# Optimization experiments

Measured on AMD Instinct MI355X. Metric: run time of the kernel, lower is better.

The kernel has to match this reference:

```python
import jax, jax.numpy as jnp
import numpy as np

B, P, K = 8, 2048, 20          # graphs, points per graph, fps samples per graph
N, M = B * P, B * K            # total points, total fps points
C_IN, C_OUT = 64, 128
EPS = 1e-5                     # BatchNorm eps (torch default)


def _linear(x, W, b):
    return x @ W.T + b


def _bn(x, g, b):
    # training-mode BatchNorm1d: batch stats over rows (biased variance)
    m = jnp.mean(x, axis=0)
    v = jnp.var(x, axis=0)
    return g * (x - m) * jax.lax.rsqrt(v + EPS) + b


def _mlp(x, W1, b1, g1, be1, W2, b2, g2, be2):
    h = jax.nn.relu(_bn(_linear(x, W1, b1), g1, be1))
    return jax.nn.relu(_bn(_linear(h, W2, b2), g2, be2))


def setup_inputs() -> dict:
    key = jax.random.key(0)
    ks = jax.random.split(key, 16)
    rng = np.random.default_rng(0)
    # sorted FPS indices: 20 distinct points per graph (matches indices.sort())
    fps = np.sort(rng.choice(P, size=(B, K), replace=False), axis=1)
    fps = fps + np.arange(B)[:, None] * P

    s = 0.05
    inp = {
        "x": jax.random.normal(ks[0], (N, C_IN), jnp.float32),
        "pos": jax.random.normal(ks[1], (N, 3), jnp.float32),
        # q/k/v projections
        "Wq": jax.random.normal(ks[2], (C_OUT, C_IN)) * s, "bq": jnp.zeros((C_OUT,)),
        "Wk": jax.random.normal(ks[3], (C_OUT, C_IN)) * s, "bk": jnp.zeros((C_OUT,)),
        "Wv": jax.random.normal(ks[4], (C_OUT, C_IN)) * s, "bv": jnp.zeros((C_OUT,)),
        # pos MLP: Linear(3,C) BN ReLU Linear(C,C) BN ReLU
        "pW1": jax.random.normal(ks[5], (C_OUT, 3)) * s, "pb1": jnp.zeros((C_OUT,)),
        "pg1": jnp.ones((C_OUT,)), "pbe1": jnp.zeros((C_OUT,)),
        "pW2": jax.random.normal(ks[6], (C_OUT, C_OUT)) * s, "pb2": jnp.zeros((C_OUT,)),
        "pg2": jnp.ones((C_OUT,)), "pbe2": jnp.zeros((C_OUT,)),
        # attn MLP: Linear(C,C) BN ReLU Linear(C,C) BN ReLU
        "aW1": jax.random.normal(ks[7], (C_OUT, C_OUT)) * s, "ab1": jnp.zeros((C_OUT,)),
        "ag1": jnp.ones((C_OUT,)), "abe1": jnp.zeros((C_OUT,)),
        "aW2": jax.random.normal(ks[8], (C_OUT, C_OUT)) * s, "ab2": jnp.zeros((C_OUT,)),
        "ag2": jnp.ones((C_OUT,)), "abe2": jnp.zeros((C_OUT,)),
        "fps_idx": jnp.asarray(fps.reshape(-1), jnp.int32),
        "batch": jnp.repeat(jnp.arange(B, dtype=jnp.int32), P),
    }
    return inp


def reference(x, pos, Wq, bq, Wk, bk, Wv, bv,
              pW1, pb1, pg1, pbe1, pW2, pb2, pg2, pbe2,
              aW1, ab1, ag1, abe1, aW2, ab2, ag2, abe2,
              fps_idx, batch):
    # --- FPS gather + knn(k=1, batched) ---
    fps_pos = pos[fps_idx]                          # [M,3]
    pos_b = pos.reshape(B, P, 3)
    fpos_b = fps_pos.reshape(B, K, 3)
    d2 = jnp.sum((pos_b[:, :, None, :] - fpos_b[:, None, :, :]) ** 2, -1)  # [B,P,K]
    nn_local = jnp.argmin(d2, axis=-1)              # [B,P] nearest fps per point
    e1 = (nn_local + jnp.arange(B)[:, None] * K).reshape(-1)  # [N] global fps idx
    ek1 = 1.0 / (1.0 + 5.0 * jnp.min(d2, axis=-1).reshape(-1))  # [N]

    # --- scatter-mean of kernel-weighted x/pos onto fps nodes ---
    seg = jax.ops.segment_sum
    cnt = jnp.maximum(seg(jnp.ones((N,), x.dtype), e1, num_segments=M), 1.0)[:, None]
    fps_x = seg(ek1[:, None] * x, e1, num_segments=M) / cnt       # [M,C_IN]
    fps_pos = seg(ek1[:, None] * pos, e1, num_segments=M) / cnt   # [M,3]

    # --- q/k/v projections ---
    x_q = _linear(x, Wq, bq)        # [N,C]
    x_k = _linear(fps_x, Wk, bk)    # [M,C]
    x_v = _linear(fps_x, Wv, bv)    # [M,C]

    # --- all-pairs (local point, global fps-in-same-graph) edges: E = N*K ---
    rel = (pos_b[:, :, None, :] - fps_pos.reshape(B, K, 3)[:, None, :, :])
    rel = rel.reshape(N * K, 3)                                   # [E,3]
    delta = _mlp(rel, pW1, pb1, pg1, pbe1, pW2, pb2, pg2, pbe2)   # [E,C]

    qmk = (x_q.reshape(B, P, 1, C_OUT) - x_k.reshape(B, 1, K, C_OUT))
    qmk = qmk.reshape(N * K, C_OUT)                               # [E,C]
    alpha = _mlp(qmk + delta, aW1, ab1, ag1, abe1, aW2, ab2, ag2, abe2)
    # segment softmax over each local point's K edges, per channel
    alpha = jax.nn.softmax(alpha.reshape(B, P, K, C_OUT), axis=2)

    vpd = x_v.reshape(B, 1, K, C_OUT) + delta.reshape(B, P, K, C_OUT)
    out = jnp.sum(vpd * alpha, axis=2).reshape(N, C_OUT)          # scatter-add
    return out
```

## Files before the change

### kernel.cpp

```cpp
#include <hip/hip_runtime.h>
#include <hip/hip_bf16.h>
#include <stdint.h>

#define B_ 8
#define P_ 2048
#define K_ 20
#define N_ (B_*P_)
#define M_ (B_*K_)
#define C 128
#define E_ (N_*K_)
#define EPS_ 1e-5f

typedef unsigned short u16;
typedef unsigned int u32;
typedef __attribute__((ext_vector_type(8))) short short8;
typedef __attribute__((ext_vector_type(4))) float floatx4;

__device__ __forceinline__ float bf2f(u16 u){
    union { u32 i; float f; } v; v.i = ((u32)u) << 16; return v.f;
}
__device__ __forceinline__ u16 f2bf(float f){
    union { float f; u32 i; } v; v.f = f;
    u32 r = ((v.i >> 16) & 1u) + 0x7fffu;
    return (u16)((v.i + r) >> 16);
}
__device__ __forceinline__ u32 pkbf(float a, float b){
    union { __hip_bfloat162 h; u32 u; } cv;
    cv.h = __float22bfloat162_rn(make_float2(a, b));
    return cv.u;
}

__global__ __launch_bounds__(256)
void prep_weights(const float* __restrict__ Wq, const float* __restrict__ bq,
                  const float* __restrict__ Wk, const float* __restrict__ bk,
                  const float* __restrict__ aW1, const float* __restrict__ ab1,
                  const float* __restrict__ pW2, const float* __restrict__ aW2,
                  float* __restrict__ Cq, float* __restrict__ Ck,
                  float* __restrict__ dq, float* __restrict__ dk,
                  u16* __restrict__ Wb0, u16* __restrict__ Wb1, u16* __restrict__ Wb2)
{
    int tid = threadIdx.x, blk = blockIdx.x;
    if (blk < 32) {
        int idx = blk*256 + tid; int o = idx >> 6, i = idx & 63;
        float s = 0.f;
        for (int cc = 0; cc < 128; ++cc) s = fmaf(aW1[o*128+cc], Wq[cc*64+i], s);
        Cq[idx] = s;
    } else if (blk < 64) {
        int idx = (blk-32)*256 + tid; int o = idx >> 6, i = idx & 63;
        float s = 0.f;
        for (int cc = 0; cc < 128; ++cc) s = fmaf(aW1[o*128+cc], Wk[cc*64+i], s);
        Ck[idx] = s;
    } else if (blk == 64) {
        if (tid < 128) {
            float s = ab1[tid];
            for (int cc = 0; cc < 128; ++cc) s = fmaf(aW1[tid*128+cc], bq[cc], s);
            dq[tid] = s;
        } else {
            int o = tid - 128;
            float s = 0.f;
            for (int cc = 0; cc < 128; ++cc) s = fmaf(aW1[o*128+cc], bk[cc], s);
            dk[o] = s;
        }
    } else {
        const float* src = (blk == 65) ? pW2 : (blk == 66) ? aW1 : aW2;
        u16* dst = (blk == 65) ? Wb0 : (blk == 66) ? Wb1 : Wb2;
        for (int s = tid; s < 2048; s += 256) {
            int ln = s & 63, ks = (s >> 6) & 3, ct = s >> 8;
            int Ls = ln & 15, qs = ln >> 4;
            const float* sp = src + (ct*16+Ls)*C + ks*32 + qs*8;
            #pragma unroll
            for (int j = 0; j < 8; ++j) dst[s*8+j] = f2bf(sp[j]);
        }
    }
}

__global__ __launch_bounds__(64)
void knn_scatter(const float* __restrict__ pos, const float* __restrict__ x,
                 const int* __restrict__ fps_idx, float* __restrict__ gacc,
                 float* __restrict__ posmom)
{
    __shared__ float fpos[K_][3];
    __shared__ float accL[K_*68];
    int lane = threadIdx.x;
    int b = blockIdx.x >> 5;
    if (lane < K_*3) {
        int k = lane / 3, d = lane - k*3;
        fpos[k][d] = pos[fps_idx[b*K_+k]*3 + d];
    }
    for (int i = lane; i < K_*68; i += 64) accL[i] = 0.f;
    __syncthreads();

    int wbase = blockIdx.x*64;
    int p = wbase + lane;
    float px = pos[p*3], py = pos[p*3+1], pz = pos[p*3+2];
    float best = 1e30f; int kb = 0;
    #pragma unroll
    for (int k = 0; k < K_; ++k) {
        float dx = px - fpos[k][0], dy = py - fpos[k][1], dz = pz - fpos[k][2];
        float d2 = dx*dx + dy*dy + dz*dz;
        if (d2 < best) { best = d2; kb = k; }
    }
    float ek = 1.0f / (1.0f + 5.0f*best);
    atomicAdd(&accL[kb*68 + 0], 1.0f);
    atomicAdd(&accL[kb*68 + 1], ek*px);
    atomicAdd(&accL[kb*68 + 2], ek*py);
    atomicAdd(&accL[kb*68 + 3], ek*pz);

    float mom[9] = {px,py,pz, px*px,px*py,px*pz, py*py,py*pz, pz*pz};
    #pragma unroll
    for (int i = 0; i < 9; ++i) {
        float v = mom[i];
        v += __shfl_xor(v,32); v += __shfl_xor(v,16); v += __shfl_xor(v,8);
        v += __shfl_xor(v,4);  v += __shfl_xor(v,2);  v += __shfl_xor(v,1);
        mom[i] = v;
    }
    if (lane == 0) {
        #pragma unroll
        for (int i = 0; i < 9; ++i) atomicAdd(&posmom[b*9+i], mom[i]);
    }

    for (int j = 0; j < 64; ++j) {
        int   kbj = __shfl(kb, j);
        float ekj = __shfl(ek, j);
        float xv = x[(size_t)(wbase+j)*64 + lane];
        atomicAdd(&accL[kbj*68 + 4 + lane], ekj*xv);
    }
    __syncthreads();
    for (int i = lane; i < K_*68; i += 64)
        atomicAdd(&gacc[b*K_*68 + i], accL[i]);
}

__global__ void fps_finalize(float* __restrict__ gacc)
{
    int m = blockIdx.x, t = threadIdx.x;
    float c = gacc[m*68]; c = c > 1.f ? c : 1.f;
    if (t >= 1 && t < 68) gacc[m*68+t] /= c;
}

__global__ __launch_bounds__(256)
void bn1_prep(const float* __restrict__ gacc, const float* __restrict__ posmom,
              const float* __restrict__ pW1, const float* __restrict__ pb1,
              const float* __restrict__ pg1, const float* __restrict__ pbe1,
              float* __restrict__ w3)
{
    __shared__ float sF[8][3], sG[8][6];
    __shared__ float S1[3], S2[6];
    int t = threadIdx.x;
    if (t < 8) {
        float F0=0,F1=0,F2=0,G0=0,G1=0,G2=0,G3=0,G4=0,G5=0;
        for (int k = 0; k < K_; ++k) {
            const float* f = gacc + (t*K_+k)*68 + 1;
            float x=f[0], y=f[1], z=f[2];
            F0+=x; F1+=y; F2+=z;
            G0+=x*x; G1+=x*y; G2+=x*z; G3+=y*y; G4+=y*z; G5+=z*z;
        }
        sF[t][0]=F0; sF[t][1]=F1; sF[t][2]=F2;
        sG[t][0]=G0; sG[t][1]=G1; sG[t][2]=G2; sG[t][3]=G3; sG[t][4]=G4; sG[t][5]=G5;
    }
    __syncthreads();
    if (t == 0) {
        float s1[3]={0,0,0}, s2[6]={0,0,0,0,0,0};
        for (int b = 0; b < 8; ++b) {
            const float* pm = posmom + b*9;
            float Ax=pm[0],Ay=pm[1],Az=pm[2];
            float Fx=sF[b][0],Fy=sF[b][1],Fz=sF[b][2];
            s1[0] += (float)K_*Ax - (float)P_*Fx;
            s1[1] += (float)K_*Ay - (float)P_*Fy;
            s1[2] += (float)K_*Az - (float)P_*Fz;
            s2[0] += (float)K_*pm[3] - 2.f*Ax*Fx + (float)P_*sG[b][0];
            s2[1] += (float)K_*pm[4] - Ax*Fy - Ay*Fx + (float)P_*sG[b][1];
            s2[2] += (float)K_*pm[5] - Ax*Fz - Az*Fx + (float)P_*sG[b][2];
            s2[3] += (float)K_*pm[6] - 2.f*Ay*Fy + (float)P_*sG[b][3];
            s2[4] += (float)K_*pm[7] - Ay*Fz - Az*Fy + (float)P_*sG[b][4];
            s2[5] += (float)K_*pm[8] - 2.f*Az*Fz + (float)P_*sG[b][5];
        }
        for (int i = 0; i < 3; ++i) S1[i] = s1[i];
        for (int i = 0; i < 6; ++i) S2[i] = s2[i];
    }
    __syncthreads();
    if (t < 128) {
        float w0=pW1[t*3], w1=pW1[t*3+1], w2=pW1[t*3+2], bb=pb1[t];
        float wS1 = w0*S1[0] + w1*S1[1] + w2*S1[2];
        float wS2w = w0*w0*S2[0] + w1*w1*S2[3] + w2*w2*S2[5]
                   + 2.f*(w0*w1*S2[1] + w0*w2*S2[2] + w1*w2*S2[4]);
        const float invE = 1.0f/(float)E_;
        float m1  = wS1*invE + bb;
        float Ez2 = (wS2w + 2.f*bb*wS1)*invE + bb*bb;
        float var = Ez2 - m1*m1;
        float sc = pg1[t] * rsqrtf(var + EPS_);
        float sh = pbe1[t] - m1*sc;
        w3[0*128+t] = w0*sc; w3[1*128+t] = w1*sc;
        w3[2*128+t] = w2*sc; w3[3*128+t] = bb*sc + sh;
    }
}

__global__ __launch_bounds__(128)
void proj_m(const float* __restrict__ gacc, const float* __restrict__ Ck,
            const float* __restrict__ dk, const float* __restrict__ Wv,
            const float* __restrict__ bv, float* __restrict__ Ak2,
            float* __restrict__ xv)
{
    int m = blockIdx.x, o = threadIdx.x;
    const float* fx = gacc + m*68 + 4;
    float a = dk[o], v = bv[o];
    for (int i = 0; i < 64; ++i) {
        float xi = fx[i];
        a = fmaf(Ck[o*64+i], xi, a);
        v = fmaf(Wv[o*64+i], xi, v);
    }
    Ak2[m*C+o] = a; xv[m*C+o] = v;
}

__global__ __launch_bounds__(256)
void proj_q(const float* __restrict__ x, const float* __restrict__ Cq,
            const float* __restrict__ dq, float* __restrict__ Aq2)
{
    __shared__ float xs[2][64];
    int tid = threadIdx.x;
    int p0 = blockIdx.x*2;
    if (tid < 128) xs[tid>>6][tid&63] = x[(p0 + (tid>>6))*64 + (tid&63)];
    __syncthreads();
    int pl = tid >> 7, o = tid & 127;
    float a = dq[o];
    const float* cq = Cq + o*64;
    const float* xr = xs[pl];
    #pragma unroll
    for (int i = 0; i < 64; i += 4) {
        a = fmaf(cq[i],   xr[i],   a);
        a = fmaf(cq[i+1], xr[i+1], a);
        a = fmaf(cq[i+2], xr[i+2], a);
        a = fmaf(cq[i+3], xr[i+3], a);
    }
    Aq2[(p0+pl)*C + o] = a;
}

__global__ __launch_bounds__(256)
void finalize_stats(const float* __restrict__ stats32,
                    const float* __restrict__ g, const float* __restrict__ be,
                    float* __restrict__ scale, float* __restrict__ shift)
{
    __shared__ float red[256];
    int tid = threadIdx.x;
    float s = 0.f;
    for (int r = 0; r < 32; ++r) s += stats32[r*256 + tid];
    red[tid] = s;
    __syncthreads();
    if (tid < C) {
        float mean = red[tid] * (1.0f/E_);
        float var  = red[C+tid] * (1.0f/E_) - mean*mean;
        float sc = g[tid] * rsqrtf(var + EPS_);
        scale[tid] = sc;
        shift[tid] = be[tid] - mean*sc;
    }
}

template<int MODE>
__global__ __launch_bounds__(256)
void gemm_fused(const u16* __restrict__ zin, u16* __restrict__ zout,
                const u16* __restrict__ Wbf,
                const float* __restrict__ scale, const float* __restrict__ shift,
                const float* __restrict__ w3,
                const float* __restrict__ bias,
                const float* __restrict__ rowq, const float* __restrict__ rowk,
                const float* __restrict__ pos, const float* __restrict__ gacc,
                float* __restrict__ stats32)
{
    __shared__ float s_stat[2][C];
    __shared__ float saff[5*C];

    int tid = threadIdx.x;
    const int wave = tid >> 6, lane = tid & 63;
    const int L = lane & 15, q = lane >> 4;

    ((float*)s_stat)[tid] = 0.f;
    if constexpr (MODE == 0) {
        for (int i = tid; i < 512; i += 256) saff[i] = w3[i];
        if (tid < C) saff[512+tid] = bias[tid];
    } else {
        if (tid < C) { saff[tid] = scale[tid]; saff[C+tid] = shift[tid]; }
        if constexpr (MODE == 2) { if (tid < C) saff[2*C+tid] = bias[tid]; }
    }
    __syncthreads();

    int tbs[2];
    tbs[0] = (blockIdx.x*8 + wave)*16;
    tbs[1] = (blockIdx.x*8 + wave + 4)*16;

    short8 An[2][4];
    float rr0[2], rr1[2], rr2[2];
    #pragma unroll
    for (int tt = 0; tt < 2; ++tt) {
        if constexpr (MODE != 0) {
            const u16* ap = zin + (size_t)(tbs[tt] + L)*C + q*8;
            An[tt][0] = *(const short8*)ap;
            An[tt][1] = *(const short8*)(ap + 32);
            An[tt][2] = *(const short8*)(ap + 64);
            An[tt][3] = *(const short8*)(ap + 96);
        } else {
            unsigned e = (unsigned)(tbs[tt] + L);
            unsigned p = e / 20u; int k = (int)(e - p*20u);
            int m = (int)(p >> 11)*20 + k;
            const float* fp = gacc + m*68 + 1;
            rr0[tt] = pos[p*3]   - fp[0];
            rr1[tt] = pos[p*3+1] - fp[1];
            rr2[tt] = pos[p*3+2] - fp[2];
        }
    }

    floatx4 acc[2][8];
    #pragma unroll
    for (int tt = 0; tt < 2; ++tt)
        #pragma unroll
        for (int ct = 0; ct < 8; ++ct) acc[tt][ct] = (floatx4){0.f,0.f,0.f,0.f};

    #pragma unroll
    for (int ks = 0; ks < 4; ++ks) {
        int ch0 = ks*32 + q*8;
        short8 bfr[8];
        #pragma unroll
        for (int ct = 0; ct < 8; ++ct)
            bfr[ct] = *(const short8*)(Wbf + ((ct*4+ks)*64 + lane)*8);
        #pragma unroll
        for (int tt = 0; tt < 2; ++tt) {
            union { short8 s8; u32 u[4]; } af;
            if constexpr (MODE == 0) {
                #pragma unroll
                for (int jj = 0; jj < 4; ++jj) {
                    int c0 = ch0 + jj*2, c1 = ch0 + jj*2 + 1;
                    float f0 = fmaf(saff[c0], rr0[tt], fmaf(saff[C+c0], rr1[tt],
                               fmaf(saff[2*C+c0], rr2[tt], saff[3*C+c0])));
                    float f1 = fmaf(saff[c1], rr0[tt], fmaf(saff[C+c1], rr1[tt],
                               fmaf(saff[2*C+c1], rr2[tt], saff[3*C+c1])));
                    f0 = f0 > 0.f ? f0 : 0.f;
                    f1 = f1 > 0.f ? f1 : 0.f;
                    af.u[jj] = pkbf(f0, f1);
                }
            } else {
                short8 ar = An[tt][ks];
                #pragma unroll
                for (int jj = 0; jj < 4; ++jj) {
                    int c0 = ch0 + jj*2, c1 = ch0 + jj*2 + 1;
                    float f0 = fmaf(bf2f((u16)ar[jj*2]),   saff[c0], saff[C+c0]);
                    float f1 = fmaf(bf2f((u16)ar[jj*2+1]), saff[c1], saff[C+c1]);
                    f0 = f0 > 0.f ? f0 : 0.f;
                    f1 = f1 > 0.f ? f1 : 0.f;
                    af.u[jj] = pkbf(f0, f1);
                }
            }
            #pragma unroll
            for (int ct = 0; ct < 8; ++ct)
                acc[tt][ct] = __builtin_amdgcn_mfma_f32_16x16x32_bf16(af.s8, bfr[ct], acc[tt][ct], 0, 0, 0);
        }
    }

    float ssum[8], ssq[8];
    #pragma unroll
    for (int i = 0; i < 8; ++i) { ssum[i] = 0.f; ssq[i] = 0.f; }

    #pragma unroll
    for (int tt = 0; tt < 2; ++tt) {
        const int tilebase = tbs[tt];
        int pp[4], mm[4];
        if constexpr (MODE == 1) {
            #pragma unroll
            for (int r = 0; r < 4; ++r) {
                unsigned e2 = (unsigned)(tilebase + q*4 + r);
                unsigned p2 = e2 / 20u; int k2 = (int)(e2 - p2*20u);
                pp[r] = (int)p2; mm[r] = (int)(p2 >> 11)*20 + k2;
            }
        }
        u16* orow = zout + (size_t)(tilebase + q*4)*C + L;
        #pragma unroll
        for (int ct = 0; ct < 8; ++ct) {
            int col = ct*16 + L;
            float bb;
            if constexpr (MODE == 0) bb = saff[4*C + col];
            else if constexpr (MODE == 2) bb = saff[2*C + col];
            else bb = 0.f;
            #pragma unroll
            for (int r = 0; r < 4; ++r) {
                float z = acc[tt][ct][r] + bb;
                if constexpr (MODE == 1)
                    z += rowq[pp[r]*C + col] - rowk[mm[r]*C + col];
                ssum[ct] += z; ssq[ct] += z*z;
                orow[(size_t)r*C + ct*16] = (u16)pkbf(z, z);
            }
        }
    }

    #pragma unroll
    for (int ct = 0; ct < 8; ++ct) {
        float v = ssum[ct]; v += __shfl_xor(v,16); v += __shfl_xor(v,32);
        float w = ssq[ct];  w += __shfl_xor(w,16); w += __shfl_xor(w,32);
        if (lane < 16) {
            atomicAdd(&s_stat[0][ct*16+L], v);
            atomicAdd(&s_stat[1][ct*16+L], w);
        }
    }
    __syncthreads();
    float* dst = stats32 + ((blockIdx.x & 31) << 8);
    atomicAdd(&dst[tid], ((float*)s_stat)[tid]);
}

__global__ __launch_bounds__(256)
void final_kernel(const u16* __restrict__ z2, const u16* __restrict__ za2,
                  const float* __restrict__ sc2, const float* __restrict__ sh2,
                  const float* __restrict__ sc4, const float* __restrict__ sh4,
                  const float* __restrict__ xv, float* __restrict__ out)
{
    int tid = threadIdx.x;
    int p = blockIdx.x*4 + (tid >> 6);
    int lane = tid & 63;
    int c2 = lane*2;
    int b = p >> 11;
    float S2x=sc2[c2], S2y=sc2[c2+1], H2x=sh2[c2], H2y=sh2[c2+1];
    float S4x=sc4[c2], S4y=sc4[c2+1], H4x=sh4[c2], H4y=sh4[c2+1];
    size_t ebase = (size_t)p * K_;
    const float* xvb = xv + (size_t)(b*K_)*C + c2;
    float l0 = 0.f, l1 = 0.f, o0 = 0.f, o1 = 0.f;
    #pragma unroll
    for (int k = 0; k < K_; ++k) {
        u32 wa = *(const u32*)(za2 + (ebase+k)*C + c2);
        u32 wz = *(const u32*)(z2  + (ebase+k)*C + c2);
        float2 xvv = *(const float2*)(xvb + (size_t)k*C);
        float aa0 = fmaf(bf2f((u16)(wa & 0xffffu)), S4x, H4x); aa0 = aa0 > 0.f ? aa0 : 0.f;
        float aa1 = fmaf(bf2f((u16)(wa >> 16)),     S4y, H4y); aa1 = aa1 > 0.f ? aa1 : 0.f;
        float dd0 = fmaf(bf2f((u16)(wz & 0xffffu)), S2x, H2x); dd0 = dd0 > 0.f ? dd0 : 0.f;
        float dd1 = fmaf(bf2f((u16)(wz >> 16)),     S2y, H2y); dd1 = dd1 > 0.f ? dd1 : 0.f;
        float e0 = __expf(aa0), e1 = __expf(aa1);
        l0 += e0; l1 += e1;
        o0 = fmaf(e0, xvv.x + dd0, o0);
        o1 = fmaf(e1, xvv.y + dd1, o1);
    }
    out[(size_t)p*C + c2]     = o0 / l0;
    out[(size_t)p*C + c2 + 1] = o1 / l1;
}

extern "C" void kernel_launch(void* const* d_in, const int* in_sizes, int n_in,
                              void* d_out, int out_size, void* d_ws, size_t ws_size,
                              hipStream_t stream)
{
    const float* x    = (const float*)d_in[0];
    const float* pos  = (const float*)d_in[1];
    const float* Wq   = (const float*)d_in[2];
    const float* bq   = (const float*)d_in[3];
    const float* Wk   = (const float*)d_in[4];
    const float* bk   = (const float*)d_in[5];
    const float* Wv   = (const float*)d_in[6];
    const float* bv   = (const float*)d_in[7];
    const float* pW1  = (const float*)d_in[8];
    const float* pb1  = (const float*)d_in[9];
    const float* pg1  = (const float*)d_in[10];
    const float* pbe1 = (const float*)d_in[11];
    const float* pW2  = (const float*)d_in[12];
    const float* pb2  = (const float*)d_in[13];
    const float* pg2  = (const float*)d_in[14];
    const float* pbe2 = (const float*)d_in[15];
    const float* aW1  = (const float*)d_in[16];
    const float* ab1  = (const float*)d_in[17];
    const float* ag1  = (const float*)d_in[18];
    const float* abe1 = (const float*)d_in[19];
    const float* aW2  = (const float*)d_in[20];
    const float* ab2  = (const float*)d_in[21];
    const float* ag2  = (const float*)d_in[22];
    const float* abe2 = (const float*)d_in[23];
    const int* fps_idx = (const int*)d_in[24];
    float* out = (float*)d_out;

    char* ws = (char*)d_ws;
    size_t off = 0;
    auto alloc = [&](size_t bytes) -> void* {
        void* r = ws + off;
        off = (off + bytes + 255) & ~(size_t)255;
        return r;
    };
    float* gacc    = (float*)alloc(160*68*4);
    float* posmom  = (float*)alloc(8*9*4);
    float* stats32 = (float*)alloc(3*32*256*4);
    size_t zero_bytes = off;
    float* aff = (float*)alloc(6*128*4);
    float* w3  = (float*)alloc(4*128*4);
    float* Cq  = (float*)alloc(128*64*4);
    float* Ck  = (float*)alloc(128*64*4);
    float* dq  = (float*)alloc(128*4);
    float* dk  = (float*)alloc(128*4);
    u16* Wb0   = (u16*)alloc(128*128*2);
    u16* Wb1   = (u16*)alloc(128*128*2);
    u16* Wb2   = (u16*)alloc(128*128*2);
    float* Aq2 = (float*)alloc((size_t)N_*128*4);
    float* Ak2 = (float*)alloc(160*128*4);
    float* xv  = (float*)alloc(160*128*4);
    u16* bigA  = (u16*)alloc((size_t)E_*128*2);
    u16* bigB  = (u16*)alloc((size_t)E_*128*2);

    hipMemsetAsync(d_ws, 0, zero_bytes, stream);

    prep_weights<<<68, 256, 0, stream>>>(Wq, bq, Wk, bk, aW1, ab1, pW2, aW2,
                                         Cq, Ck, dq, dk, Wb0, Wb1, Wb2);
    knn_scatter<<<256, 64, 0, stream>>>(pos, x, fps_idx, gacc, posmom);
    fps_finalize<<<160, 128, 0, stream>>>(gacc);
    bn1_prep<<<1, 256, 0, stream>>>(gacc, posmom, pW1, pb1, pg1, pbe1, w3);
    proj_m<<<160, 128, 0, stream>>>(gacc, Ck, dk, Wv, bv, Ak2, xv);
    proj_q<<<N_/2, 256, 0, stream>>>(x, Cq, dq, Aq2);

    float* stA = stats32;
    float* stB = stats32 + 32*256;
    float* stC = stats32 + 2*32*256;

    gemm_fused<0><<<E_/128, 256, 0, stream>>>(nullptr, bigA, Wb0,
        nullptr, nullptr, w3, pb2, nullptr, nullptr, pos, gacc, stA);
    finalize_stats<<<1, 256, 0, stream>>>(stA, pg2, pbe2, aff + 0, aff + 128);

    gemm_fused<1><<<E_/128, 256, 0, stream>>>(bigA, bigB, Wb1,
        aff + 0, aff + 128, nullptr, nullptr, Aq2, Ak2, nullptr, nullptr, stB);
    finalize_stats<<<1, 256, 0, stream>>>(stB, ag1, abe1, aff + 256, aff + 384);

    gemm_fused<2><<<E_/128, 256, 0, stream>>>(bigB, bigB, Wb2,
        aff + 256, aff + 384, nullptr, ab2, nullptr, nullptr, nullptr, nullptr, stC);
    finalize_stats<<<1, 256, 0, stream>>>(stC, ag2, abe2, aff + 512, aff + 640);

    final_kernel<<<N_/4, 256, 0, stream>>>(bigA, bigB, aff + 0, aff + 128,
                                           aff + 512, aff + 640, xv, out);
}
```

Measured before the change: 387.4 us.

## Transpose projection weights and widen knn_scatter and proj_q blocks

The fused query/key weights and Wv are now written transposed, so threads indexed by output channel read consecutive addresses and loads coalesce. proj_q now handles 8 points per block with 4 accumulators per thread, reusing each weight load across 4 points. knn_scatter grows to 256 threads and splits the x scatter loop across 4 waves, with kb/ek passed through shared memory instead of shuffles. The risks are more LDS atomic contention on accL and one extra prep block for the Wv transpose.

After: 333.7 us. 1.16x faster.

```diff
diff --git a/kernel.cpp b/kernel.cpp
--- a/kernel.cpp
+++ b/kernel.cpp
@@ -35,8 +35,10 @@
                   const float* __restrict__ Wk, const float* __restrict__ bk,
                   const float* __restrict__ aW1, const float* __restrict__ ab1,
                   const float* __restrict__ pW2, const float* __restrict__ aW2,
-                  float* __restrict__ Cq, float* __restrict__ Ck,
+                  const float* __restrict__ Wv,
+                  float* __restrict__ CqT, float* __restrict__ CkT,
                   float* __restrict__ dq, float* __restrict__ dk,
+                  float* __restrict__ WvT,
                   u16* __restrict__ Wb0, u16* __restrict__ Wb1, u16* __restrict__ Wb2)
 {
     int tid = threadIdx.x, blk = blockIdx.x;
@@ -44,12 +46,12 @@
         int idx = blk*256 + tid; int o = idx >> 6, i = idx & 63;
         float s = 0.f;
         for (int cc = 0; cc < 128; ++cc) s = fmaf(aW1[o*128+cc], Wq[cc*64+i], s);
-        Cq[idx] = s;
+        CqT[i*128 + o] = s;
     } else if (blk < 64) {
         int idx = (blk-32)*256 + tid; int o = idx >> 6, i = idx & 63;
         float s = 0.f;
         for (int cc = 0; cc < 128; ++cc) s = fmaf(aW1[o*128+cc], Wk[cc*64+i], s);
-        Ck[idx] = s;
+        CkT[i*128 + o] = s;
     } else if (blk == 64) {
         if (tid < 128) {
             float s = ab1[tid];
@@ -61,6 +63,11 @@
             for (int cc = 0; cc < 128; ++cc) s = fmaf(aW1[o*128+cc], bk[cc], s);
             dk[o] = s;
         }
+    } else if (blk == 68) {
+        for (int idx = tid; idx < 8192; idx += 256) {
+            int o = idx >> 6, i = idx & 63;
+            WvT[i*128 + o] = Wv[idx];
+        }
     } else {
         const float* src = (blk == 65) ? pW2 : (blk == 66) ? aW1 : aW2;
         u16* dst = (blk == 65) ? Wb0 : (blk == 66) ? Wb1 : Wb2;
@@ -74,59 +81,68 @@
     }
 }
 
-__global__ __launch_bounds__(64)
+__global__ __launch_bounds__(256)
 void knn_scatter(const float* __restrict__ pos, const float* __restrict__ x,
                  const int* __restrict__ fps_idx, float* __restrict__ gacc,
                  float* __restrict__ posmom)
 {
     __shared__ float fpos[K_][3];
     __shared__ float accL[K_*68];
-    int lane = threadIdx.x;
+    __shared__ int   skb[64];
+    __shared__ float sek[64];
+    int tid = threadIdx.x;
     int b = blockIdx.x >> 5;
-    if (lane < K_*3) {
-        int k = lane / 3, d = lane - k*3;
+    if (tid < K_*3) {
+        int k = tid / 3, d = tid - k*3;
         fpos[k][d] = pos[fps_idx[b*K_+k]*3 + d];
     }
-    for (int i = lane; i < K_*68; i += 64) accL[i] = 0.f;
+    for (int i = tid; i < K_*68; i += 256) accL[i] = 0.f;
     __syncthreads();
 
     int wbase = blockIdx.x*64;
-    int p = wbase + lane;
-    float px = pos[p*3], py = pos[p*3+1], pz = pos[p*3+2];
-    float best = 1e30f; int kb = 0;
-    #pragma unroll
-    for (int k = 0; k < K_; ++k) {
-        float dx = px - fpos[k][0], dy = py - fpos[k][1], dz = pz - fpos[k][2];
-        float d2 = dx*dx + dy*dy + dz*dz;
-        if (d2 < best) { best = d2; kb = k; }
-    }
-    float ek = 1.0f / (1.0f + 5.0f*best);
-    atomicAdd(&accL[kb*68 + 0], 1.0f);
-    atomicAdd(&accL[kb*68 + 1], ek*px);
-    atomicAdd(&accL[kb*68 + 2], ek*py);
-    atomicAdd(&accL[kb*68 + 3], ek*pz);
-
-    float mom[9] = {px,py,pz, px*px,px*py,px*pz, py*py,py*pz, pz*pz};
-    #pragma unroll
-    for (int i = 0; i < 9; ++i) {
-        float v = mom[i];
-        v += __shfl_xor(v,32); v += __shfl_xor(v,16); v += __shfl_xor(v,8);
-        v += __shfl_xor(v,4);  v += __shfl_xor(v,2);  v += __shfl_xor(v,1);
-        mom[i] = v;
-    }
-    if (lane == 0) {
+    if (tid < 64) {
+        int p = wbase + tid;
+        float px = pos[p*3], py = pos[p*3+1], pz = pos[p*3+2];
+        float best = 1e30f; int kb = 0;
         #pragma unroll
-        for (int i = 0; i < 9; ++i) atomicAdd(&posmom[b*9+i], mom[i]);
-    }
-
-    for (int j = 0; j < 64; ++j) {
-        int   kbj = __shfl(kb, j);
-        float ekj = __shfl(ek, j);
+        for (int k = 0; k < K_; ++k) {
+            float dx = px - fpos[k][0], dy = py - fpos[k][1], dz = pz - fpos[k][2];
+            float d2 = dx*dx + dy*dy + dz*dz;
+            if (d2 < best) { best = d2; kb = k; }
+        }
+        float ek = 1.0f / (1.0f + 5.0f*best);
+        skb[tid] = kb; sek[tid] = ek;
+        atomicAdd(&accL[kb*68 + 0], 1.0f);
+        atomicAdd(&accL[kb*68 + 1], ek*px);
+        atomicAdd(&accL[kb*68 + 2], ek*py);
+        atomicAdd(&accL[kb*68 + 3], ek*pz);
+
+        float mom[9] = {px,py,pz, px*px,px*py,px*pz, py*py,py*pz, pz*pz};
+        #pragma unroll
+        for (int i = 0; i < 9; ++i) {
+            float v = mom[i];
+            v += __shfl_xor(v,32); v += __shfl_xor(v,16); v += __shfl_xor(v,8);
+            v += __shfl_xor(v,4);  v += __shfl_xor(v,2);  v += __shfl_xor(v,1);
+            mom[i] = v;
+        }
+        if (tid == 0) {
+            #pragma unroll
+            for (int i = 0; i < 9; ++i) atomicAdd(&posmom[b*9+i], mom[i]);
+        }
+    }
+    __syncthreads();
+
+    int w = tid >> 6, lane = tid & 63;
+    #pragma unroll
+    for (int jj = 0; jj < 16; ++jj) {
+        int j = w*16 + jj;
+        int   kbj = skb[j];
+        float ekj = sek[j];
         float xv = x[(size_t)(wbase+j)*64 + lane];
         atomicAdd(&accL[kbj*68 + 4 + lane], ekj*xv);
     }
     __syncthreads();
-    for (int i = lane; i < K_*68; i += 64)
+    for (int i = tid; i < K_*68; i += 256)
         atomicAdd(&gacc[b*K_*68 + i], accL[i]);
 }
 
@@ -195,8 +211,8 @@
 }
 
 __global__ __launch_bounds__(128)
-void proj_m(const float* __restrict__ gacc, const float* __restrict__ Ck,
-            const float* __restrict__ dk, const float* __restrict__ Wv,
+void proj_m(const float* __restrict__ gacc, const float* __restrict__ CkT,
+            const float* __restrict__ dk, const float* __restrict__ WvT,
             const float* __restrict__ bv, float* __restrict__ Ak2,
             float* __restrict__ xv)
 {
@@ -205,33 +221,39 @@
     float a = dk[o], v = bv[o];
     for (int i = 0; i < 64; ++i) {
         float xi = fx[i];
-        a = fmaf(Ck[o*64+i], xi, a);
-        v = fmaf(Wv[o*64+i], xi, v);
+        a = fmaf(CkT[i*128+o], xi, a);
+        v = fmaf(WvT[i*128+o], xi, v);
     }
     Ak2[m*C+o] = a; xv[m*C+o] = v;
 }
 
 __global__ __launch_bounds__(256)
-void proj_q(const float* __restrict__ x, const float* __restrict__ Cq,
+void proj_q(const float* __restrict__ x, const float* __restrict__ CqT,
             const float* __restrict__ dq, float* __restrict__ Aq2)
 {
-    __shared__ float xs[2][64];
+    __shared__ float xs[512];
     int tid = threadIdx.x;
-    int p0 = blockIdx.x*2;
-    if (tid < 128) xs[tid>>6][tid&63] = x[(p0 + (tid>>6))*64 + (tid&63)];
-    __syncthreads();
-    int pl = tid >> 7, o = tid & 127;
-    float a = dq[o];
-    const float* cq = Cq + o*64;
-    const float* xr = xs[pl];
-    #pragma unroll
-    for (int i = 0; i < 64; i += 4) {
-        a = fmaf(cq[i],   xr[i],   a);
-        a = fmaf(cq[i+1], xr[i+1], a);
-        a = fmaf(cq[i+2], xr[i+2], a);
-        a = fmaf(cq[i+3], xr[i+3], a);
-    }
-    Aq2[(p0+pl)*C + o] = a;
+    int p0 = blockIdx.x*8;
+    const float* xp = x + (size_t)p0*64;
+    for (int i = tid; i < 512; i += 256) xs[i] = xp[i];
+    __syncthreads();
+    int g = tid >> 7, o = tid & 127;
+    const float* xb = xs + g*256;
+    float d = dq[o];
+    float a0=d, a1=d, a2=d, a3=d;
+    #pragma unroll 4
+    for (int i = 0; i < 64; ++i) {
+        float w = CqT[i*128 + o];
+        a0 = fmaf(w, xb[i],       a0);
+        a1 = fmaf(w, xb[64+i],    a1);
+        a2 = fmaf(w, xb[128+i],   a2);
+        a3 = fmaf(w, xb[192+i],   a3);
+    }
+    int pb = p0 + g*4;
+    Aq2[(size_t)(pb+0)*C + o] = a0;
+    Aq2[(size_t)(pb+1)*C + o] = a1;
+    Aq2[(size_t)(pb+2)*C + o] = a2;
+    Aq2[(size_t)(pb+3)*C + o] = a3;
 }
 
 __global__ __launch_bounds__(256)
@@ -480,10 +502,11 @@
     size_t zero_bytes = off;
     float* aff = (float*)alloc(6*128*4);
     float* w3  = (float*)alloc(4*128*4);
-    float* Cq  = (float*)alloc(128*64*4);
-    float* Ck  = (float*)alloc(128*64*4);
+    float* CqT = (float*)alloc(64*128*4);
+    float* CkT = (float*)alloc(64*128*4);
     float* dq  = (float*)alloc(128*4);
     float* dk  = (float*)alloc(128*4);
+    float* WvT = (float*)alloc(64*128*4);
     u16* Wb0   = (u16*)alloc(128*128*2);
     u16* Wb1   = (u16*)alloc(128*128*2);
     u16* Wb2   = (u16*)alloc(128*128*2);
@@ -495,13 +518,13 @@
 
     hipMemsetAsync(d_ws, 0, zero_bytes, stream);
 
-    prep_weights<<<68, 256, 0, stream>>>(Wq, bq, Wk, bk, aW1, ab1, pW2, aW2,
-                                         Cq, Ck, dq, dk, Wb0, Wb1, Wb2);
-    knn_scatter<<<256, 64, 0, stream>>>(pos, x, fps_idx, gacc, posmom);
+    prep_weights<<<69, 256, 0, stream>>>(Wq, bq, Wk, bk, aW1, ab1, pW2, aW2, Wv,
+                                         CqT, CkT, dq, dk, WvT, Wb0, Wb1, Wb2);
+    knn_scatter<<<256, 256, 0, stream>>>(pos, x, fps_idx, gacc, posmom);
     fps_finalize<<<160, 128, 0, stream>>>(gacc);
     bn1_prep<<<1, 256, 0, stream>>>(gacc, posmom, pW1, pb1, pg1, pbe1, w3);
-    proj_m<<<160, 128, 0, stream>>>(gacc, Ck, dk, Wv, bv, Ak2, xv);
-    proj_q<<<N_/2, 256, 0, stream>>>(x, Cq, dq, Aq2);
+    proj_m<<<160, 128, 0, stream>>>(gacc, CkT, dk, WvT, bv, Ak2, xv);
+    proj_q<<<N_/8, 256, 0, stream>>>(x, CqT, dq, Aq2);
 
     float* stA = stats32;
     float* stB = stats32 + 32*256;
```
